# Optimization experiments

Hardware: AMD Instinct MI355X
Metric: run time of the kernel (lower is better)

Reference implementation:

```python
import jax, jax.numpy as jnp
import numpy as np

# OPT-1.3b-like attention dims
B, S, E, NH, HD = 1, 2048, 2048, 32, 64
Q_BITS, R_BITS, BASE_GS, R_GS = 1, 3, 16, 16


def quotrem_fake_quantize(x, q_bits=Q_BITS, r_bits=R_BITS, base_gs=BASE_GS, r_gs=R_GS):
    r_max = 2 ** (r_bits - 1) - 1
    r_min = -r_max - 1
    eps = 1e-8
    shape = x.shape
    H = shape[-1]
    xg = x.reshape(shape[:-1] + (H // base_gs, base_gs))  # [..., G_base, base_gs]
    max_abs = jnp.maximum(jnp.max(jnp.abs(xg), axis=-1, keepdims=True), eps)
    if q_bits == 1:
        log2_max = jnp.log2(max_abs)
        base_floor = jnp.exp2(jnp.floor(log2_max))
        base_ceil = jnp.exp2(jnp.ceil(log2_max))
        base = jnp.where(jnp.abs(max_abs - base_floor) <= jnp.abs(base_ceil - max_abs),
                         base_floor, base_ceil)
        base = jnp.clip(base, 1.0, 128.0)
        max_pos = jnp.max(xg, axis=-1, keepdims=True)
        min_val = jnp.min(xg, axis=-1, keepdims=True)
        sign_flag = jnp.where(jnp.abs(max_pos) >= jnp.abs(min_val), 1.0, -1.0)
        q = (xg * sign_flag >= base / 2.0).astype(x.dtype)
        q_scaled = q * sign_flag * base
    else:
        q_max = 2 ** (q_bits - 1) - 1
        threshold = max_abs / q_max
        base = jnp.full_like(threshold, 64.0)
        for b in (32.0, 16.0, 8.0, 4.0, 2.0):
            base = jnp.where(threshold <= b, jnp.full_like(threshold, b), base)
        q = jnp.clip(jnp.round(xg / base), -q_max, q_max)
        q_scaled = q * base
    r = (xg - q_scaled).reshape(shape)
    rg = r.reshape(shape[:-1] + (H // r_gs, r_gs))  # [..., G_r, r_gs]
    max_abs_r = jnp.maximum(jnp.max(jnp.abs(rg), axis=-1, keepdims=True), eps)
    scale_r = max_abs_r / r_max
    r_q = jnp.clip(jnp.round(rg / scale_r), r_min, r_max)
    r_dq = (r_q * scale_r).reshape(shape)
    return q_scaled.reshape(shape) + r_dq


def setup_inputs() -> dict:
    key = jax.random.key(0)
    ks = jax.random.split(key, 9)
    w = lambda k: jax.random.normal(k, (E, E), dtype=jnp.float32) * 0.02
    b = lambda k: jax.random.normal(k, (E,), dtype=jnp.float32) * 0.02
    return {
        "hidden_states": jax.random.normal(ks[0], (B, S, E), dtype=jnp.float32),
        "Wq": w(ks[1]), "bq": b(ks[2]),
        "Wk": w(ks[3]), "bk": b(ks[4]),
        "Wv": w(ks[5]), "bv": b(ks[6]),
        "Wo": w(ks[7]), "bo": b(ks[8]),
    }


def reference(hidden_states, Wq, bq, Wk, bk, Wv, bv, Wo, bo):
    scaling = HD ** -0.5
    heads = lambda x: x.reshape(B, S, NH, HD).transpose(0, 2, 1, 3)  # [B,NH,S,HD]
    q = heads((hidden_states @ Wq.T + bq) * scaling)
    k = quotrem_fake_quantize(heads(hidden_states @ Wk.T + bk))
    v = quotrem_fake_quantize(heads(hidden_states @ Wv.T + bv))
    scores = jnp.einsum('bhqd,bhkd->bhqk', q, k)
    idx = jnp.arange(S)
    scores = jnp.where(idx[:, None] >= idx[None, :], scores, -jnp.inf)  # causal
    attn = jax.nn.softmax(scores, axis=-1)
    out = jnp.einsum('bhqk,bhkd->bhqd', attn, v).transpose(0, 2, 1, 3).reshape(B, S, E)
    return out @ Wo.T + bo
```

## Files before the change

kernel.cpp:

```cpp
#include <hip/hip_runtime.h>
#include <math.h>

#define SEQ 2048
#define EMB 2048
#define NHEAD 32
#define HDIM 64

typedef unsigned short u16;
typedef _Float16 half8 __attribute__((ext_vector_type(8)));
typedef _Float16 half4 __attribute__((ext_vector_type(4)));
typedef __attribute__((ext_vector_type(4))) float floatx4;

__device__ __forceinline__ floatx4 mfma_f16(half8 a, half8 b, floatx4 c) {
    return __builtin_amdgcn_mfma_f32_16x16x32_f16(a, b, c, 0, 0, 0);
}
__device__ __forceinline__ void load16(const u16* g, u16* l) {
    __builtin_amdgcn_global_load_lds(
        (const __attribute__((address_space(1))) unsigned int*)g,
        (__attribute__((address_space(3))) unsigned int*)l, 16, 0, 0);
}
__device__ __forceinline__ u16 h2u(_Float16 h) { return *reinterpret_cast<u16*>(&h); }

__global__ __launch_bounds__(256)
void cvt4(const float* __restrict__ X0, u16* __restrict__ Y0,
          const float* __restrict__ X1, u16* __restrict__ Y1,
          const float* __restrict__ X2, u16* __restrict__ Y2,
          const float* __restrict__ X3, u16* __restrict__ Y3)
{
    const float* Xs[4] = {X0, X1, X2, X3};
    u16* Ys[4] = {Y0, Y1, Y2, Y3};
    const float* X = Xs[blockIdx.y];
    u16* Y = Ys[blockIdx.y];
    const int i = (blockIdx.x * 256 + threadIdx.x) * 4;
    float4 v = *reinterpret_cast<const float4*>(X + i);
    half4 hv;
    hv.x = (_Float16)v.x; hv.y = (_Float16)v.y;
    hv.z = (_Float16)v.z; hv.w = (_Float16)v.w;
    *reinterpret_cast<half4*>(Y + i) = hv;
}

__global__ __launch_bounds__(512, 2)
void gemm256(const u16* __restrict__ A,
             const u16* __restrict__ B0, const u16* __restrict__ B1,
             const u16* __restrict__ B2,
             const float* __restrict__ bk, const float* __restrict__ bv,
             const float* __restrict__ bq,
             float* __restrict__ F0, float* __restrict__ F1,
             u16* __restrict__ Qb)
{
    __shared__ __align__(16) u16 As[2][256 * 64];
    __shared__ __align__(16) u16 Bs[2][256 * 64];

    const int tid = threadIdx.x;
    const int w = tid >> 6, lane = tid & 63;
    const int wm = w >> 2, wn = w & 3;
    const int quad = lane >> 4, colk = lane & 15;
    const int lrow = lane >> 3, lphy = lane & 7;
    const int lsLog = (lphy - lrow) & 7;
    const int bn = blockIdx.x, bm = blockIdx.y, z = blockIdx.z;

    const u16* Bg  = (z == 0) ? B0 : (z == 1) ? B1 : B2;
    const u16* Ag  = A  + (size_t)(bm * 256 + lrow) * EMB + lsLog * 8;
    const u16* Bgp = Bg + (size_t)(bn * 256 + lrow) * EMB + lsLog * 8;

    const int kp0 = ((quad + colk) & 7) * 8;
    const int kp1 = ((quad + 4 + colk) & 7) * 8;
    int arow[8], brow[4];
    #pragma unroll
    for (int i = 0; i < 8; ++i) arow[i] = (wm * 128 + 16 * i + colk) * 64;
    #pragma unroll
    for (int j = 0; j < 4; ++j) brow[j] = (wn * 64 + 16 * j + colk) * 64;

    floatx4 acc[8][4];
    #pragma unroll
    for (int i = 0; i < 8; ++i)
        #pragma unroll
        for (int j = 0; j < 4; ++j) acc[i][j] = (floatx4){0.f, 0.f, 0.f, 0.f};

#define STAGE_A(MQ, BUF, KT) {                                                \
    _Pragma("unroll") for (int p_ = 0; p_ < 2; ++p_) {                        \
        const int r0_ = 128 * p_ + (MQ) * 64 + w * 8;                         \
        load16(Ag + (size_t)r0_ * EMB + (KT), &As[BUF][r0_ * 64 + lane * 8]); \
    } }
#define STAGE_B(NQ, BUF, KT) {                                                \
    _Pragma("unroll") for (int p_ = 0; p_ < 2; ++p_) {                        \
        const int b_ = w + 8 * p_;                                            \
        const int r0_ = 64 * (b_ >> 2) + (NQ) * 32 + (b_ & 3) * 8;            \
        load16(Bgp + (size_t)r0_ * EMB + (KT), &Bs[BUF][r0_ * 64 + lane * 8]);\
    } }

#define PHASE(MQ, NQ, BUF, STAGE, GUARD) {                                    \
    half8 af[4][2], bf[2][2];                                                 \
    _Pragma("unroll") for (int ii = 0; ii < 4; ++ii) {                        \
        const u16* ap_ = &As[BUF][arow[4 * (MQ) + ii]];                       \
        af[ii][0] = *reinterpret_cast<const half8*>(ap_ + kp0);               \
        af[ii][1] = *reinterpret_cast<const half8*>(ap_ + kp1);               \
    }                                                                         \
    _Pragma("unroll") for (int jj = 0; jj < 2; ++jj) {                        \
        const u16* bp_ = &Bs[BUF][brow[2 * (NQ) + jj]];                       \
        bf[jj][0] = *reinterpret_cast<const half8*>(bp_ + kp0);               \
        bf[jj][1] = *reinterpret_cast<const half8*>(bp_ + kp1);               \
    }                                                                         \
    STAGE                                                                     \
    __builtin_amdgcn_s_barrier();                                             \
    asm volatile("s_waitcnt lgkmcnt(0)" ::: "memory");                        \
    __builtin_amdgcn_s_setprio(1);                                            \
    _Pragma("unroll") for (int ii = 0; ii < 4; ++ii)                          \
        _Pragma("unroll") for (int jj = 0; jj < 2; ++jj) {                    \
            acc[4*(MQ)+ii][2*(NQ)+jj] =                                       \
                mfma_f16(af[ii][0], bf[jj][0], acc[4*(MQ)+ii][2*(NQ)+jj]);    \
            acc[4*(MQ)+ii][2*(NQ)+jj] =                                       \
                mfma_f16(af[ii][1], bf[jj][1], acc[4*(MQ)+ii][2*(NQ)+jj]);    \
        }                                                                     \
    __builtin_amdgcn_s_setprio(0);                                            \
    if (GUARD) asm volatile("s_waitcnt vmcnt(4)" ::: "memory");               \
    __builtin_amdgcn_s_barrier();                                             \
    __builtin_amdgcn_sched_barrier(0);                                        \
}

    STAGE_B(0, 0, 0)
    STAGE_A(0, 0, 0)
    STAGE_A(1, 0, 0)
    STAGE_B(1, 0, 0)
    STAGE_B(0, 1, 64)
    STAGE_A(0, 1, 64)
    asm volatile("s_waitcnt vmcnt(4)" ::: "memory");
    __builtin_amdgcn_s_barrier();
    __builtin_amdgcn_sched_barrier(0);

    #pragma unroll 1
    for (int it = 0; it < 16; ++it) {
        const int k1 = ((2 * it + 1) & 31) * 64;
        const int k2 = ((2 * it + 2) & 31) * 64;
        const int k3 = ((2 * it + 3) & 31) * 64;
        PHASE(0, 0, 0, STAGE_A(1, 1, k1), 0)
        PHASE(1, 0, 0, STAGE_B(1, 1, k1), 0)
        PHASE(0, 1, 0, STAGE_B(0, 0, k2), 0)
        PHASE(1, 1, 0, STAGE_A(0, 0, k2), 1)
        PHASE(0, 0, 1, STAGE_A(1, 0, k2), 0)
        PHASE(1, 0, 1, STAGE_B(1, 0, k2), 0)
        PHASE(0, 1, 1, STAGE_B(0, 1, k3), 0)
        PHASE(1, 1, 1, STAGE_A(0, 1, k3), 1)
    }
    asm volatile("s_waitcnt vmcnt(0)" ::: "memory");

#undef STAGE_A
#undef STAGE_B
#undef PHASE

    const float* bias = (z == 0) ? bk : (z == 1) ? bv : bq;
    #pragma unroll
    for (int i = 0; i < 8; ++i) {
        const int row = bm * 256 + wm * 128 + 16 * i + 4 * quad;
        #pragma unroll
        for (int j = 0; j < 4; ++j) {
            const int col = bn * 256 + wn * 64 + 16 * j + colk;
            const float bb = bias[col];
            #pragma unroll
            for (int r = 0; r < 4; ++r) {
                const size_t idx = (size_t)(row + r) * EMB + col;
                if (z == 2)
                    ((_Float16*)Qb)[idx] = (_Float16)((acc[i][j][r] + bb) * 0.125f);
                else
                    ((z == 0) ? F0 : F1)[idx] = acc[i][j][r] + bb;
            }
        }
    }
}

__global__ __launch_bounds__(256)
void gemm16(const u16* __restrict__ A,
            const u16* __restrict__ B0, const u16* __restrict__ B1,
            const u16* __restrict__ B2,
            const float* __restrict__ bk, const float* __restrict__ bv,
            const float* __restrict__ bq,
            float* __restrict__ F0, float* __restrict__ F1,
            u16* __restrict__ Qb)
{
    __shared__ __align__(16) u16 As[128 * 64];
    __shared__ __align__(16) u16 Bs[128 * 64];

    const int tid = threadIdx.x;
    const int w = tid >> 6, lane = tid & 63;
    const int quad = lane >> 4, colk = lane & 15;
    const int bn = blockIdx.x, bm = blockIdx.y, z = blockIdx.z;
    const int wm = (w & 1) * 64, wn = (w >> 1) * 64;

    const u16* Bg = (z == 0) ? B0 : (z == 1) ? B1 : B2;

    const int srow = tid >> 3, sphy = tid & 7;
    const int sLog = (sphy - srow) & 7;
    size_t agof[4], bgof[4];
    int ldst[4];
    #pragma unroll
    for (int p = 0; p < 4; ++p) {
        const int row = srow + 32 * p;
        agof[p] = (size_t)(bm * 128 + row) * EMB + sLog * 8;
        bgof[p] = (size_t)(bn * 128 + row) * EMB + sLog * 8;
        ldst[p] = (tid + 256 * p) * 8;
    }

    const int aoct0 = ((quad + colk) & 7) * 8;
    const int aoct1 = ((quad + 4 + colk) & 7) * 8;

    floatx4 acc[4][4];
    #pragma unroll
    for (int i = 0; i < 4; ++i)
        #pragma unroll
        for (int j = 0; j < 4; ++j) acc[i][j] = (floatx4){0.f, 0.f, 0.f, 0.f};

    for (int kt = 0; kt < 2048; kt += 64) {
        __syncthreads();
        #pragma unroll
        for (int p = 0; p < 4; ++p) {
            load16(A  + agof[p] + kt, As + ldst[p]);
            load16(Bg + bgof[p] + kt, Bs + ldst[p]);
        }
        __syncthreads();

        half8 a0[4], a1[4], b0[4], b1[4];
        #pragma unroll
        for (int i = 0; i < 4; ++i) {
            a0[i] = *reinterpret_cast<const half8*>(&As[(wm + 16*i + colk) * 64 + aoct0]);
            a1[i] = *reinterpret_cast<const half8*>(&As[(wm + 16*i + colk) * 64 + aoct1]);
        }
        #pragma unroll
        for (int j = 0; j < 4; ++j) {
            b0[j] = *reinterpret_cast<const half8*>(&Bs[(wn + 16*j + colk) * 64 + aoct0]);
            b1[j] = *reinterpret_cast<const half8*>(&Bs[(wn + 16*j + colk) * 64 + aoct1]);
        }
        #pragma unroll
        for (int i = 0; i < 4; ++i)
            #pragma unroll
            for (int j = 0; j < 4; ++j) {
                acc[i][j] = mfma_f16(a0[i], b0[j], acc[i][j]);
                acc[i][j] = mfma_f16(a1[i], b1[j], acc[i][j]);
            }
    }

    const float* bias = (z == 0) ? bk : (z == 1) ? bv : bq;
    #pragma unroll
    for (int i = 0; i < 4; ++i) {
        const int row = bm * 128 + wm + 16*i + 4*quad;
        #pragma unroll
        for (int j = 0; j < 4; ++j) {
            const int col = bn * 128 + wn + 16*j + colk;
            const float bv2 = bias[col];
            #pragma unroll
            for (int r = 0; r < 4; ++r) {
                const size_t idx = (size_t)(row + r) * EMB + col;
                if (z == 2)
                    ((_Float16*)Qb)[idx] = (_Float16)((acc[i][j][r] + bv2) * 0.125f);
                else
                    ((z == 0) ? F0 : F1)[idx] = acc[i][j][r] + bv2;
            }
        }
    }
}

__device__ __forceinline__ void quotrem16(float* x)
{
    float maxabs = 1e-8f, maxpos = -INFINITY, minval = INFINITY;
    #pragma unroll
    for (int i = 0; i < 16; ++i) {
        maxabs = fmaxf(maxabs, fabsf(x[i]));
        maxpos = fmaxf(maxpos, x[i]);
        minval = fminf(minval, x[i]);
    }
    const float lg = log2f(maxabs);
    const float bfl = exp2f(floorf(lg));
    const float bcl = exp2f(ceilf(lg));
    float base = (fabsf(maxabs - bfl) <= fabsf(bcl - maxabs)) ? bfl : bcl;
    base = fminf(fmaxf(base, 1.0f), 128.0f);
    const float sgn = (fabsf(maxpos) >= fabsf(minval)) ? 1.0f : -1.0f;
    const float hb = 0.5f * base, sb = sgn * base;

    float qs[16], r[16], maxr = 1e-8f;
    #pragma unroll
    for (int i = 0; i < 16; ++i) {
        qs[i] = (x[i] * sgn >= hb) ? sb : 0.0f;
        r[i]  = x[i] - qs[i];
        maxr  = fmaxf(maxr, fabsf(r[i]));
    }
    const float scale = maxr / 3.0f;
    #pragma unroll
    for (int i = 0; i < 16; ++i) {
        float rq = rintf(r[i] / scale);
        rq = fminf(fmaxf(rq, -4.0f), 3.0f);
        x[i] = qs[i] + rq * scale;
    }
}

__global__ __launch_bounds__(256)
void quant_kv(const float* __restrict__ FK, u16* __restrict__ Kb,
              const float* __restrict__ FV, u16* __restrict__ Vt,
              const float* __restrict__ Wo, u16* __restrict__ Wo16)
{
    __shared__ u16 T[64 * 264];
    const int bid = blockIdx.x, t = threadIdx.x;

    if (bid >= 1280) {
        const int i = ((bid - 1280) * 256 + t) * 4;
        float4 v = *reinterpret_cast<const float4*>(Wo + i);
        half4 hv;
        hv.x = (_Float16)v.x; hv.y = (_Float16)v.y;
        hv.z = (_Float16)v.z; hv.w = (_Float16)v.w;
        *reinterpret_cast<half4*>(Wo16 + i) = hv;
        return;
    }

    if (bid < 1024) {
        const int g = bid * 256 + t;
        const float* p = FK + (size_t)g * 16;
        float x[16];
        #pragma unroll
        for (int i = 0; i < 16; i += 4)
            *reinterpret_cast<float4*>(&x[i]) = *reinterpret_cast<const float4*>(p + i);
        quotrem16(x);
        _Float16* o = (_Float16*)Kb + (size_t)g * 16;
        #pragma unroll
        for (int i = 0; i < 16; ++i) o[i] = (_Float16)x[i];
        return;
    }

    const int l = bid - 1024;
    const int sb = l >> 5, h = l & 31;
    const float* src = FV + (size_t)(sb * 256 + t) * EMB + h * HDIM;

    #pragma unroll
    for (int g4 = 0; g4 < 4; ++g4) {
        float x[16];
        #pragma unroll
        for (int i = 0; i < 16; i += 4)
            *reinterpret_cast<float4*>(&x[i]) =
                *reinterpret_cast<const float4*>(src + g4 * 16 + i);
        quotrem16(x);
        #pragma unroll
        for (int i = 0; i < 16; ++i)
            T[(g4 * 16 + i) * 264 + t] = h2u((_Float16)x[i]);
    }
    __syncthreads();

    const int d = t >> 2, seg = t & 3;
    u16* dst = Vt + (size_t)(h * HDIM + d) * SEQ + sb * 256 + seg * 64;
    #pragma unroll
    for (int jj = 0; jj < 8; ++jj)
        *reinterpret_cast<half8*>(dst + jj * 8) =
            *reinterpret_cast<const half8*>(&T[d * 264 + seg * 64 + jj * 8]);
}

__global__ __launch_bounds__(256)
void flash128(const u16* __restrict__ Qb, const u16* __restrict__ Kb,
              const u16* __restrict__ Vt, u16* __restrict__ Ob)
{
    __shared__ __align__(16) u16 Ks[128 * 64];
    __shared__ __align__(16) u16 Vs[64 * 128];
    __shared__ __align__(16) u16 Ps[64 * 136];

    const int tid = threadIdx.x;
    const int w = tid >> 6, lane = tid & 63;
    const int quad = lane >> 4, colk = lane & 15;
    const int id = blockIdx.x;
    const int h = (id & 7) * 4 + ((id >> 3) & 3);
    const int pairb = id >> 5;

    int krow[4], koff[4], vd[4], voff[4];
    #pragma unroll
    for (int p = 0; p < 4; ++p) {
        const int c = tid + p * 256;
        krow[p] = c >> 3;
        koff[p] = (((c & 7) - krow[p]) & 7) * 8;
        vd[p]   = c >> 4;
        voff[p] = (((c & 15) - vd[p]) & 15) * 8;
    }
    const int ldb0 = w * 512;
    const int kp0 = ((quad + colk) & 7) * 8;
    const int kp1 = ((quad + 4 + colk) & 7) * 8;

    #pragma unroll
    for (int pass = 0; pass < 2; ++pass) {
        const int qt = pass ? (31 - pairb) : pairb;
        const int nw = (qt + 2) >> 1;
        const int qrow_g = qt * 64 + 16 * w + colk;

        __syncthreads();
        #pragma unroll
        for (int p = 0; p < 2; ++p) {
            const int c = tid + p * 256, row = c >> 3, cq = c & 7;
            *reinterpret_cast<half8*>(&Ps[row * 136 + cq * 8]) =
                *reinterpret_cast<const half8*>(&Qb[(size_t)(qt * 64 + row) * EMB + h * HDIM + cq * 8]);
        }
        __syncthreads();
        const half8 qb0 = *reinterpret_cast<const half8*>(&Ps[(16*w + colk) * 136 + quad * 8]);
        const half8 qb1 = *reinterpret_cast<const half8*>(&Ps[(16*w + colk) * 136 + 32 + quad * 8]);

        floatx4 o[4];
        #pragma unroll
        for (int t = 0; t < 4; ++t) o[t] = (floatx4){0.f, 0.f, 0.f, 0.f};
        float lsum = 0.f;

        for (int kw = 0; kw < nw; ++kw) {
            __syncthreads();
            #pragma unroll
            for (int p = 0; p < 4; ++p) {
                load16(Kb + (size_t)(kw * 128 + krow[p]) * EMB + h * HDIM + koff[p],
                       Ks + p * 2048 + ldb0);
                load16(Vt + (size_t)(h * HDIM + vd[p]) * SEQ + kw * 128 + voff[p],
                       Vs + p * 2048 + ldb0);
            }
            __syncthreads();

            floatx4 s[8];
            #pragma unroll
            for (int t = 0; t < 8; ++t) {
                const half8 kb0 = *reinterpret_cast<const half8*>(&Ks[(16*t + colk) * 64 + kp0]);
                const half8 kb1 = *reinterpret_cast<const half8*>(&Ks[(16*t + colk) * 64 + kp1]);
                floatx4 zz = (floatx4){0.f, 0.f, 0.f, 0.f};
                zz = mfma_f16(kb0, qb0, zz);
                s[t] = mfma_f16(kb1, qb1, zz);
            }
            if (kw == nw - 1) {
                #pragma unroll
                for (int t = 0; t < 8; ++t)
                    #pragma unroll
                    for (int r = 0; r < 4; ++r)
                        if (kw * 128 + 16*t + 4*quad + r > qrow_g) s[t][r] = -INFINITY;
            }

            #pragma unroll
            for (int t = 0; t < 8; ++t) {
                half4 pw;
                float pv0 = __expf(s[t][0] - 4.0f), pv1 = __expf(s[t][1] - 4.0f);
                float pv2 = __expf(s[t][2] - 4.0f), pv3 = __expf(s[t][3] - 4.0f);
                lsum += (pv0 + pv1) + (pv2 + pv3);
                pw.x = (_Float16)pv0; pw.y = (_Float16)pv1;
                pw.z = (_Float16)pv2; pw.w = (_Float16)pv3;
                *reinterpret_cast<half4*>(&Ps[(16*w + colk) * 136 + 16*t + 4*quad]) = pw;
            }

            half8 pa[4];
            #pragma unroll
            for (int seg = 0; seg < 4; ++seg)
                pa[seg] = *reinterpret_cast<const half8*>(&Ps[(16*w + colk) * 136 + seg * 32 + quad * 8]);
            #pragma unroll
            for (int t = 0; t < 4; ++t) {
                #pragma unroll
                for (int seg = 0; seg < 4; ++seg) {
                    const int vp = ((4*seg + quad + colk) & 15) * 8;
                    const half8 vb = *reinterpret_cast<const half8*>(&Vs[(16*t + colk) * 128 + vp]);
                    o[t] = mfma_f16(pa[seg], vb, o[t]);
                }
            }
        }

        lsum += __shfl_xor(lsum, 16, 64);
        lsum += __shfl_xor(lsum, 32, 64);

        float invr[4];
        #pragma unroll
        for (int r = 0; r < 4; ++r) invr[r] = 1.0f / __shfl(lsum, 4*quad + r, 64);
        #pragma unroll
        for (int t = 0; t < 4; ++t)
            #pragma unroll
            for (int r = 0; r < 4; ++r) {
                const int row = qt * 64 + 16*w + 4*quad + r;
                ((_Float16*)Ob)[(size_t)row * EMB + h * HDIM + 16*t + colk] =
                    (_Float16)(o[t][r] * invr[r]);
            }
    }
}

extern "C" void kernel_launch(void* const* d_in, const int* in_sizes, int n_in,
                              void* d_out, int out_size, void* d_ws, size_t ws_size,
                              hipStream_t stream)
{
    const float* hidden = (const float*)d_in[0];
    const float* Wq = (const float*)d_in[1];
    const float* bq = (const float*)d_in[2];
    const float* Wk = (const float*)d_in[3];
    const float* bk = (const float*)d_in[4];
    const float* Wv = (const float*)d_in[5];
    const float* bv = (const float*)d_in[6];
    const float* Wo = (const float*)d_in[7];
    const float* bo = (const float*)d_in[8];
    float* out = (float*)d_out;

    char* ws = (char*)d_ws;
    const size_t MB = 1024 * 1024;
    u16*   H16  = (u16*)(ws);
    u16*   Wk16 = (u16*)(ws + 8 * MB);
    u16*   Wv16 = (u16*)(ws + 16 * MB);
    float* FK   = (float*)(ws + 24 * MB);
    float* FV   = (float*)(ws + 40 * MB);
    u16*   Qbuf = (u16*)(ws + 56 * MB);
    u16*   Kbuf = (u16*)(ws + 8 * MB);
    u16*   Vtb  = (u16*)(ws + 16 * MB);
    u16*   Wo16 = (u16*)(ws);
    u16*   Obuf = (u16*)(ws + 24 * MB);
    u16*   Wq16 = (u16*)d_out;

    const dim3 cb(256);
    float* nilf = nullptr; u16* nil16 = nullptr;

    hipLaunchKernelGGL(cvt4, dim3(4096, 4), cb, 0, stream,
                       hidden, H16, Wk, Wk16, Wv, Wv16, Wq, Wq16);
    hipLaunchKernelGGL(gemm256, dim3(8, 8, 3), dim3(512), 0, stream,
                       H16, Wk16, Wv16, Wq16, bk, bv, bq, FK, FV, Qbuf);
    hipLaunchKernelGGL(quant_kv, dim3(1280 + 4096), cb, 0, stream,
                       FK, Kbuf, FV, Vtb, Wo, Wo16);
    hipLaunchKernelGGL(flash128, dim3(512), cb, 0, stream,
                       Qbuf, Kbuf, Vtb, Obuf);
    hipLaunchKernelGGL(gemm16, dim3(16, 16, 1), cb, 0, stream,
                       Obuf, Wo16, nil16, nil16, bo, nilf, nilf,
                       out, nilf, nil16);
}
```

Baseline: 298.3 us.

## Reorder QKV GEMM phases to reuse fragments and peel the final iteration

```diff
diff --git a/kernel.cpp b/kernel.cpp
--- a/kernel.cpp
+++ b/kernel.cpp
@@ -76,6 +76,8 @@
     for (int i = 0; i < 8; ++i)
         #pragma unroll
         for (int j = 0; j < 4; ++j) acc[i][j] = (floatx4){0.f, 0.f, 0.f, 0.f};
+
+    half8 af[4][2], bf0[2][2], bf1[2][2];
 
 #define STAGE_A(MQ, BUF, KT) {                                                \
     _Pragma("unroll") for (int p_ = 0; p_ < 2; ++p_) {                        \
@@ -88,64 +90,79 @@
         const int r0_ = 64 * (b_ >> 2) + (NQ) * 32 + (b_ & 3) * 8;            \
         load16(Bgp + (size_t)r0_ * EMB + (KT), &Bs[BUF][r0_ * 64 + lane * 8]);\
     } }
-
-#define PHASE(MQ, NQ, BUF, STAGE, GUARD) {                                    \
-    half8 af[4][2], bf[2][2];                                                 \
-    _Pragma("unroll") for (int ii = 0; ii < 4; ++ii) {                        \
-        const u16* ap_ = &As[BUF][arow[4 * (MQ) + ii]];                       \
-        af[ii][0] = *reinterpret_cast<const half8*>(ap_ + kp0);               \
-        af[ii][1] = *reinterpret_cast<const half8*>(ap_ + kp1);               \
-    }                                                                         \
-    _Pragma("unroll") for (int jj = 0; jj < 2; ++jj) {                        \
-        const u16* bp_ = &Bs[BUF][brow[2 * (NQ) + jj]];                       \
-        bf[jj][0] = *reinterpret_cast<const half8*>(bp_ + kp0);               \
-        bf[jj][1] = *reinterpret_cast<const half8*>(bp_ + kp1);               \
-    }                                                                         \
+#define READ_A(MQ, BUF)                                                       \
+    _Pragma("unroll") for (int ii_ = 0; ii_ < 4; ++ii_) {                     \
+        const u16* ap_ = &As[BUF][arow[4*(MQ)+ii_]];                          \
+        af[ii_][0] = *reinterpret_cast<const half8*>(ap_ + kp0);              \
+        af[ii_][1] = *reinterpret_cast<const half8*>(ap_ + kp1);              \
+    }
+#define READ_B(NQ, BUF, DST)                                                  \
+    _Pragma("unroll") for (int jj_ = 0; jj_ < 2; ++jj_) {                     \
+        const u16* bp_ = &Bs[BUF][brow[2*(NQ)+jj_]];                          \
+        DST[jj_][0] = *reinterpret_cast<const half8*>(bp_ + kp0);             \
+        DST[jj_][1] = *reinterpret_cast<const half8*>(bp_ + kp1);             \
+    }
+#define VM6 asm volatile("s_waitcnt vmcnt(6)" ::: "memory");
+#define VM8 asm volatile("s_waitcnt vmcnt(8)" ::: "memory");
+#define VM0 asm volatile("s_waitcnt vmcnt(0)" ::: "memory");
+
+#define PHASE(READS, STAGE, MQ, NQ, BF, GUARD, NEEDLGKM) {                    \
+    READS                                                                     \
     STAGE                                                                     \
     __builtin_amdgcn_s_barrier();                                             \
-    asm volatile("s_waitcnt lgkmcnt(0)" ::: "memory");                        \
+    if (NEEDLGKM) {                                                           \
+        asm volatile("s_waitcnt lgkmcnt(0)" ::: "memory");                    \
+        __builtin_amdgcn_sched_barrier(0);                                    \
+    }                                                                         \
     __builtin_amdgcn_s_setprio(1);                                            \
     _Pragma("unroll") for (int ii = 0; ii < 4; ++ii)                          \
         _Pragma("unroll") for (int jj = 0; jj < 2; ++jj) {                    \
             acc[4*(MQ)+ii][2*(NQ)+jj] =                                       \
-                mfma_f16(af[ii][0], bf[jj][0], acc[4*(MQ)+ii][2*(NQ)+jj]);    \
+                mfma_f16(af[ii][0], BF[jj][0], acc[4*(MQ)+ii][2*(NQ)+jj]);    \
             acc[4*(MQ)+ii][2*(NQ)+jj] =                                       \
-                mfma_f16(af[ii][1], bf[jj][1], acc[4*(MQ)+ii][2*(NQ)+jj]);    \
+                mfma_f16(af[ii][1], BF[jj][1], acc[4*(MQ)+ii][2*(NQ)+jj]);    \
         }                                                                     \
     __builtin_amdgcn_s_setprio(0);                                            \
-    if (GUARD) asm volatile("s_waitcnt vmcnt(4)" ::: "memory");               \
+    GUARD                                                                     \
     __builtin_amdgcn_s_barrier();                                             \
     __builtin_amdgcn_sched_barrier(0);                                        \
 }
 
-    STAGE_B(0, 0, 0)
-    STAGE_A(0, 0, 0)
-    STAGE_A(1, 0, 0)
-    STAGE_B(1, 0, 0)
-    STAGE_B(0, 1, 64)
-    STAGE_A(0, 1, 64)
-    asm volatile("s_waitcnt vmcnt(4)" ::: "memory");
+    STAGE_A(0, 0, 0)  STAGE_B(0, 0, 0)  STAGE_B(1, 0, 0)  STAGE_A(1, 0, 0)
+    STAGE_A(0, 1, 64) STAGE_B(0, 1, 64) STAGE_B(1, 1, 64) STAGE_A(1, 1, 64)
+    asm volatile("s_waitcnt vmcnt(8)" ::: "memory");
     __builtin_amdgcn_s_barrier();
     __builtin_amdgcn_sched_barrier(0);
 
     #pragma unroll 1
-    for (int it = 0; it < 16; ++it) {
-        const int k1 = ((2 * it + 1) & 31) * 64;
-        const int k2 = ((2 * it + 2) & 31) * 64;
-        const int k3 = ((2 * it + 3) & 31) * 64;
-        PHASE(0, 0, 0, STAGE_A(1, 1, k1), 0)
-        PHASE(1, 0, 0, STAGE_B(1, 1, k1), 0)
-        PHASE(0, 1, 0, STAGE_B(0, 0, k2), 0)
-        PHASE(1, 1, 0, STAGE_A(0, 0, k2), 1)
-        PHASE(0, 0, 1, STAGE_A(1, 0, k2), 0)
-        PHASE(1, 0, 1, STAGE_B(1, 0, k2), 0)
-        PHASE(0, 1, 1, STAGE_B(0, 1, k3), 0)
-        PHASE(1, 1, 1, STAGE_A(0, 1, k3), 1)
-    }
-    asm volatile("s_waitcnt vmcnt(0)" ::: "memory");
+    for (int it = 0; it < 15; ++it) {
+        const int k2 = (2 * it + 2) * 64;
+        const int k3 = (2 * it + 3) * 64;
+        PHASE(READ_A(0,0) READ_B(0,0,bf0), {},                0,0,bf0, {},  1)
+        PHASE(READ_B(1,0,bf1),             STAGE_A(0,0,k2),   0,1,bf1, {},  1)
+        PHASE(READ_A(1,0),                 STAGE_B(0,0,k2),   1,1,bf1, {},  1)
+        PHASE({},                          STAGE_B(1,0,k2),   1,0,bf0, VM6, 0)
+        PHASE(READ_A(0,1) READ_B(0,1,bf0), STAGE_A(1,0,k2),   0,0,bf0, {},  1)
+        PHASE(READ_B(1,1,bf1),             STAGE_A(0,1,k3),   0,1,bf1, {},  1)
+        PHASE(READ_A(1,1),                 STAGE_B(0,1,k3),   1,1,bf1, {},  1)
+        PHASE({},    STAGE_B(1,1,k3) STAGE_A(1,1,k3),         1,0,bf0, VM8, 0)
+    }
+    PHASE(READ_A(0,0) READ_B(0,0,bf0), {}, 0,0,bf0, {},  1)
+    PHASE(READ_B(1,0,bf1),             {}, 0,1,bf1, {},  1)
+    PHASE(READ_A(1,0),                 {}, 1,1,bf1, {},  1)
+    PHASE({},                          {}, 1,0,bf0, VM0, 0)
+    PHASE(READ_A(0,1) READ_B(0,1,bf0), {}, 0,0,bf0, {},  1)
+    PHASE(READ_B(1,1,bf1),             {}, 0,1,bf1, {},  1)
+    PHASE(READ_A(1,1),                 {}, 1,1,bf1, {},  1)
+    PHASE({},                          {}, 1,0,bf0, {},  0)
 
 #undef STAGE_A
 #undef STAGE_B
+#undef READ_A
+#undef READ_B
+#undef VM6
+#undef VM8
+#undef VM0
 #undef PHASE
 
     const float* bias = (z == 0) ? bk : (z == 1) ? bv : bq;
```

Result: faster. 287.0 us (-3.8%).

## Double-buffer K/V tiles and widen flash blocks to 128 query rows

Applied to the files above, without the earlier changes.

```diff
diff --git a/kernel.cpp b/kernel.cpp
--- a/kernel.cpp
+++ b/kernel.cpp
@@ -349,72 +349,79 @@
             *reinterpret_cast<const half8*>(&T[d * 264 + seg * 64 + jj * 8]);
 }
 
-__global__ __launch_bounds__(256)
+__global__ __launch_bounds__(512)
 void flash128(const u16* __restrict__ Qb, const u16* __restrict__ Kb,
               const u16* __restrict__ Vt, u16* __restrict__ Ob)
 {
-    __shared__ __align__(16) u16 Ks[128 * 64];
-    __shared__ __align__(16) u16 Vs[64 * 128];
-    __shared__ __align__(16) u16 Ps[64 * 136];
+    __shared__ __align__(16) u16 Ks[2][128 * 64];
+    __shared__ __align__(16) u16 Vs[2][64 * 128];
+    __shared__ __align__(16) u16 Ps[128 * 136];
 
     const int tid = threadIdx.x;
     const int w = tid >> 6, lane = tid & 63;
+    const int wg = w >> 2, wl = w & 3;
     const int quad = lane >> 4, colk = lane & 15;
     const int id = blockIdx.x;
     const int h = (id & 7) * 4 + ((id >> 3) & 3);
     const int pairb = id >> 5;
 
-    int krow[4], koff[4], vd[4], voff[4];
-    #pragma unroll
-    for (int p = 0; p < 4; ++p) {
-        const int c = tid + p * 256;
+    int krow[2], koff[2], vd[2], voff[2], ldst[2];
+    #pragma unroll
+    for (int p = 0; p < 2; ++p) {
+        const int c = tid + p * 512;
         krow[p] = c >> 3;
         koff[p] = (((c & 7) - krow[p]) & 7) * 8;
         vd[p]   = c >> 4;
         voff[p] = (((c & 15) - vd[p]) & 15) * 8;
-    }
-    const int ldb0 = w * 512;
+        ldst[p] = c * 8;
+    }
     const int kp0 = ((quad + colk) & 7) * 8;
     const int kp1 = ((quad + 4 + colk) & 7) * 8;
+    const int rloc = wg * 64 + 16 * wl + colk;
+
+#define STAGEKV(KW, BUF) {                                                     \
+    _Pragma("unroll") for (int p_ = 0; p_ < 2; ++p_) {                         \
+        load16(Kb + (size_t)((KW) * 128 + krow[p_]) * EMB + h * HDIM + koff[p_],\
+               &Ks[BUF][ldst[p_]]);                                            \
+        load16(Vt + (size_t)(h * HDIM + vd[p_]) * SEQ + (KW) * 128 + voff[p_], \
+               &Vs[BUF][ldst[p_]]);                                            \
+    } }
 
     #pragma unroll
     for (int pass = 0; pass < 2; ++pass) {
-        const int qt = pass ? (31 - pairb) : pairb;
-        const int nw = (qt + 2) >> 1;
-        const int qrow_g = qt * 64 + 16 * w + colk;
-
-        __syncthreads();
-        #pragma unroll
-        for (int p = 0; p < 2; ++p) {
-            const int c = tid + p * 256, row = c >> 3, cq = c & 7;
-            *reinterpret_cast<half8*>(&Ps[row * 136 + cq * 8]) =
-                *reinterpret_cast<const half8*>(&Qb[(size_t)(qt * 64 + row) * EMB + h * HDIM + cq * 8]);
-        }
-        __syncthreads();
-        const half8 qb0 = *reinterpret_cast<const half8*>(&Ps[(16*w + colk) * 136 + quad * 8]);
-        const half8 qb1 = *reinterpret_cast<const half8*>(&Ps[(16*w + colk) * 136 + 32 + quad * 8]);
+        const int qt = pass ? (15 - pairb) : pairb;
+        const int nw = qt + 1;
+        const int qrow_g = qt * 128 + rloc;
+
+        const half8 qb0 = *reinterpret_cast<const half8*>(
+            &Qb[(size_t)qrow_g * EMB + h * HDIM + quad * 8]);
+        const half8 qb1 = *reinterpret_cast<const half8*>(
+            &Qb[(size_t)qrow_g * EMB + h * HDIM + 32 + quad * 8]);
+
+        STAGEKV(0, 0)
 
         floatx4 o[4];
         #pragma unroll
         for (int t = 0; t < 4; ++t) o[t] = (floatx4){0.f, 0.f, 0.f, 0.f};
         float lsum = 0.f;
-
+        int cur = 0;
+
+        #pragma unroll 1
         for (int kw = 0; kw < nw; ++kw) {
-            __syncthreads();
-            #pragma unroll
-            for (int p = 0; p < 4; ++p) {
-                load16(Kb + (size_t)(kw * 128 + krow[p]) * EMB + h * HDIM + koff[p],
-                       Ks + p * 2048 + ldb0);
-                load16(Vt + (size_t)(h * HDIM + vd[p]) * SEQ + kw * 128 + voff[p],
-                       Vs + p * 2048 + ldb0);
-            }
-            __syncthreads();
+            if (kw + 1 < nw) {
+                STAGEKV(kw + 1, cur ^ 1)
+                asm volatile("s_waitcnt vmcnt(4)" ::: "memory");
+            } else {
+                asm volatile("s_waitcnt vmcnt(0)" ::: "memory");
+            }
+            __builtin_amdgcn_s_barrier();
+            __builtin_amdgcn_sched_barrier(0);
 
             floatx4 s[8];
             #pragma unroll
             for (int t = 0; t < 8; ++t) {
-                const half8 kb0 = *reinterpret_cast<const half8*>(&Ks[(16*t + colk) * 64 + kp0]);
-                const half8 kb1 = *reinterpret_cast<const half8*>(&Ks[(16*t + colk) * 64 + kp1]);
+                const half8 kb0 = *reinterpret_cast<const half8*>(&Ks[cur][(16*t + colk) * 64 + kp0]);
+                const half8 kb1 = *reinterpret_cast<const half8*>(&Ks[cur][(16*t + colk) * 64 + kp1]);
                 floatx4 zz = (floatx4){0.f, 0.f, 0.f, 0.f};
                 zz = mfma_f16(kb0, qb0, zz);
                 s[t] = mfma_f16(kb1, qb1, zz);
@@ -435,22 +442,26 @@
                 lsum += (pv0 + pv1) + (pv2 + pv3);
                 pw.x = (_Float16)pv0; pw.y = (_Float16)pv1;
                 pw.z = (_Float16)pv2; pw.w = (_Float16)pv3;
-                *reinterpret_cast<half4*>(&Ps[(16*w + colk) * 136 + 16*t + 4*quad]) = pw;
+                *reinterpret_cast<half4*>(&Ps[rloc * 136 + 16*t + 4*quad]) = pw;
             }
 
             half8 pa[4];
             #pragma unroll
             for (int seg = 0; seg < 4; ++seg)
-                pa[seg] = *reinterpret_cast<const half8*>(&Ps[(16*w + colk) * 136 + seg * 32 + quad * 8]);
+                pa[seg] = *reinterpret_cast<const half8*>(&Ps[rloc * 136 + seg * 32 + quad * 8]);
             #pragma unroll
             for (int t = 0; t < 4; ++t) {
                 #pragma unroll
                 for (int seg = 0; seg < 4; ++seg) {
                     const int vp = ((4*seg + quad + colk) & 15) * 8;
-                    const half8 vb = *reinterpret_cast<const half8*>(&Vs[(16*t + colk) * 128 + vp]);
+                    const half8 vb = *reinterpret_cast<const half8*>(&Vs[cur][(16*t + colk) * 128 + vp]);
                     o[t] = mfma_f16(pa[seg], vb, o[t]);
                 }
             }
+
+            __builtin_amdgcn_s_barrier();
+            __builtin_amdgcn_sched_barrier(0);
+            cur ^= 1;
         }
 
         lsum += __shfl_xor(lsum, 16, 64);
@@ -463,11 +474,12 @@
         for (int t = 0; t < 4; ++t)
             #pragma unroll
             for (int r = 0; r < 4; ++r) {
-                const int row = qt * 64 + 16*w + 4*quad + r;
+                const int row = qt * 128 + wg * 64 + 16*wl + 4*quad + r;
                 ((_Float16*)Ob)[(size_t)row * EMB + h * HDIM + 16*t + colk] =
                     (_Float16)(o[t][r] * invr[r]);
             }
     }
+#undef STAGEKV
 }
 
 extern "C" void kernel_launch(void* const* d_in, const int* in_sizes, int n_in,
@@ -508,7 +520,7 @@
                        H16, Wk16, Wv16, Wq16, bk, bv, bq, FK, FV, Qbuf);
     hipLaunchKernelGGL(quant_kv, dim3(1280 + 4096), cb, 0, stream,
                        FK, Kbuf, FV, Vtb, Wo, Wo16);
-    hipLaunchKernelGGL(flash128, dim3(512), cb, 0, stream,
+    hipLaunchKernelGGL(flash128, dim3(256), dim3(512), 0, stream,
                        Qbuf, Kbuf, Vtb, Obuf);
     hipLaunchKernelGGL(gemm16, dim3(16, 16, 1), cb, 0, stream,
                        Obuf, Wo16, nil16, nil16, bo, nilf, nilf,
```

Result: no change. 295.7 us (-0.8%).
